# Kernel optimization log

Hardware: AMD Instinct MI355X
Metric: run time of the kernel (lower is better)

## Reference

```python
import jax, jax.numpy as jnp
import numpy as np


def gatv2(x, src, dst, ea, Wl, bl, Wr, br, We, att, bias, N):
    # PyG GATv2Conv: source/target projections, edge embedding, leaky_relu(0.2)
    # attention, segment softmax over incoming edges, scatter-add aggregation.
    H, C = att.shape
    xl = (x @ Wl.T + bl).reshape(-1, H, C)   # [N,H,C] (source / message features)
    xr = (x @ Wr.T + br).reshape(-1, H, C)   # [N,H,C] (target features)
    ee = (ea @ We.T).reshape(-1, H, C)       # [E,H,C] edge embedding
    e = jax.nn.leaky_relu(xl[src] + xr[dst] + ee, 0.2)   # [E,H,C]
    s = jnp.einsum('ehc,hc->eh', e, att)                  # [E,H] scores
    smax = jax.ops.segment_max(s, dst, num_segments=N)
    ex = jnp.exp(s - smax[dst])
    den = jax.ops.segment_sum(ex, dst, num_segments=N)
    a = ex / (den[dst] + 1e-16)                           # segment softmax
    out = jax.ops.segment_sum(a[:, :, None] * xl[src], dst, num_segments=N)
    return out.reshape(N, H * C) + bias


def _forward(x, edge_index, edge_attr, actions, Wl1, bl1, Wr1, br1, We1, att1, bias1,
             Wl2, bl2, Wr2, br2, We2, att2, bias2, Wf, bf, Wp, bp, alpha):
    N = x.shape[0]
    E = edge_attr.shape[0]
    num_actions = E + 1
    src, dst = edge_index[0], edge_index[1]
    # add_self_loops(fill_value='mean'): self-loop edge_attr = per-node mean of incoming edge_attr
    cnt = jax.ops.segment_sum(jnp.ones((E,), x.dtype), dst, num_segments=N)
    mean_ea = jax.ops.segment_sum(edge_attr, dst, num_segments=N) / jnp.maximum(cnt, 1.0)[:, None]
    loop = jnp.arange(N, dtype=src.dtype)
    src2 = jnp.concatenate([src, loop])
    dst2 = jnp.concatenate([dst, loop])
    ea2 = jnp.concatenate([edge_attr, mean_ea], axis=0)
    h = jax.nn.relu(gatv2(x, src2, dst2, ea2, Wl1, bl1, Wr1, br1, We1, att1, bias1, N))
    h = jax.nn.relu(gatv2(h, src2, dst2, ea2, Wl2, bl2, Wr2, br2, We2, att2, bias2, N))
    g = jnp.mean(h, axis=0, keepdims=True)              # global_mean_pool, single graph -> [1,hid]
    state_potential = jax.nn.relu(g @ Wp.T + bp)[:, 0]  # [1]
    diag = jnp.concatenate([src != dst, jnp.array([True])])  # [E+1]
    logits = (g @ Wf.T + bf)[:, :num_actions]           # [1, E+1]
    amask = jnp.ones((num_actions,), bool).at[actions].set(False)
    mask = amask & diag
    logits = jnp.where(mask[None, :], logits, -jnp.inf)
    return jax.nn.softmax(logits, axis=1), state_potential, jax.nn.sigmoid(alpha)


def setup_inputs() -> dict:
    key = jax.random.key(0)
    ks = jax.random.split(key, 16)
    N, E, F, hid, H, A = 20000, 400000, 128, 64, 4, 450000
    x = jax.random.normal(ks[0], (N, F), jnp.float32)
    src = jax.random.randint(ks[1], (E,), 0, N)
    dst = (src + 1 + jax.random.randint(ks[2], (E,), 0, N - 1)) % N  # no pre-existing self loops
    edge_index = jnp.stack([src, dst])
    edge_attr = jax.random.normal(ks[3], (E, 1), jnp.float32)
    actions = jax.random.randint(ks[4], (128,), 0, E + 1)
    s = 0.05
    nrm = lambda k, shp: jax.random.normal(k, shp, jnp.float32) * s
    return {
        'x': x, 'edge_index': edge_index, 'edge_attr': edge_attr, 'actions': actions,
        'Wl1': nrm(ks[5], (H * hid, F)), 'bl1': jnp.zeros(H * hid),
        'Wr1': nrm(ks[6], (H * hid, F)), 'br1': jnp.zeros(H * hid),
        'We1': nrm(ks[7], (H * hid, 1)), 'att1': nrm(ks[8], (H, hid)), 'bias1': jnp.zeros(H * hid),
        'Wl2': nrm(ks[9], (hid, H * hid)), 'bl2': jnp.zeros(hid),
        'Wr2': nrm(ks[10], (hid, H * hid)), 'br2': jnp.zeros(hid),
        'We2': nrm(ks[11], (hid, 1)), 'att2': nrm(ks[12], (1, hid)), 'bias2': jnp.zeros(hid),
        'Wf': nrm(ks[13], (A, hid)), 'bf': jnp.zeros(A),
        'Wp': nrm(ks[14], (1, hid)), 'bp': jnp.zeros(1),
        'alpha': jnp.asarray(0.0, jnp.float32),
    }


def reference(x, edge_index, edge_attr, actions, Wl1, bl1, Wr1, br1, We1, att1, bias1,
              Wl2, bl2, Wr2, br2, We2, att2, bias2, Wf, bf, Wp, bp, alpha):
    return _forward(x, edge_index, edge_attr, actions, Wl1, bl1, Wr1, br1, We1, att1, bias1,
                    Wl2, bl2, Wr2, br2, We2, att2, bias2, Wf, bf, Wp, bp, alpha)
```

## Files before the change

kernel.cpp:

```cpp
#include <hip/hip_runtime.h>
#include <math.h>

typedef __attribute__((ext_vector_type(8))) short short8;
typedef __attribute__((ext_vector_type(4))) float f32x4;

__device__ __forceinline__ float wred_sum(float v) {
#pragma unroll
  for (int off = 32; off; off >>= 1) v += __shfl_xor(v, off, 64);
  return v;
}
__device__ __forceinline__ float wred_max(float v) {
#pragma unroll
  for (int off = 32; off; off >>= 1) v = fmaxf(v, __shfl_xor(v, off, 64));
  return v;
}
__device__ __forceinline__ unsigned f2key(float x) {
  unsigned b = __float_as_uint(x);
  return (b & 0x80000000u) ? ~b : (b | 0x80000000u);
}
__device__ __forceinline__ float key2f(unsigned k) {
  unsigned b = (k & 0x80000000u) ? (k & 0x7FFFFFFFu) : ~k;
  return __uint_as_float(b);
}
__device__ __forceinline__ float b2f(unsigned short u) {
  return __uint_as_float(((unsigned)u) << 16);
}
__device__ __forceinline__ unsigned short f2b(float f) {
  unsigned b = __float_as_uint(f);
  return (unsigned short)((b + 0x7FFFu + ((b >> 16) & 1u)) >> 16);
}

__global__ __launch_bounds__(256) void k_prep(
    const float* __restrict__ s0, ushort* __restrict__ d0, int n0,
    const float* __restrict__ s1, ushort* __restrict__ d1, int n1,
    const float* __restrict__ s2, ushort* __restrict__ d2, int n2,
    const float* __restrict__ s3, ushort* __restrict__ d3, int n3,
    const float* __restrict__ s4, ushort* __restrict__ d4, int n4,
    const int* __restrict__ dstv, const float* __restrict__ ea,
    int* __restrict__ cnt_i, float* __restrict__ sum_ea, int E,
    const int* __restrict__ actions, unsigned char* __restrict__ aflag,
    int n_act, int castB) {
  int b = blockIdx.x, tid = threadIdx.x;
  if (b == 0 && tid < n_act) aflag[actions[tid]] = 1;
  if (b < castB) {
    int t = (b * 256 + tid) * 4;
    const float* s; ushort* d; int off = t;
    if (off < n0) { s = s0; d = d0; }
    else { off -= n0;
      if (off < n1) { s = s1; d = d1; }
      else { off -= n1;
        if (off < n2) { s = s2; d = d2; }
        else { off -= n2;
          if (off < n3) { s = s3; d = d3; }
          else { off -= n3;
            if (off < n4) { s = s4; d = d4; }
            else return; } } } }
    float4 v = *(const float4*)(s + off);
    ushort4 o;
    o.x = f2b(v.x); o.y = f2b(v.y); o.z = f2b(v.z); o.w = f2b(v.w);
    *(ushort4*)(d + off) = o;
    return;
  }
  int e = (b - castB) * 256 + tid;
  if (e >= E) return;
  int d = dstv[e];
  atomicAdd(&cnt_i[d], 1);
  atomicAdd(&sum_ea[d], ea[e]);
}

__global__ __launch_bounds__(1024) void k_scan(const int* __restrict__ cnt_i,
    const float* __restrict__ sum_ea, float* __restrict__ mean_ea,
    int* __restrict__ row_st, int* __restrict__ cursor, int N) {
  __shared__ int ws[16];
  int tid = threadIdx.x;
  int lane = tid & 63, w = tid >> 6;
  int running = 0;
  for (int base = 0; base < N; base += 1024) {
    int i = base + tid;
    int c = 0;
    if (i < N) {
      int cc = cnt_i[i];
      c = cc + 1;
      mean_ea[i] = sum_ea[i] / fmaxf((float)cc, 1.0f);
    }
    int inc = c;
#pragma unroll
    for (int off = 1; off < 64; off <<= 1) {
      int u = __shfl_up(inc, off, 64);
      if (lane >= off) inc += u;
    }
    if (lane == 63) ws[w] = inc;
    __syncthreads();
    if (tid < 16) {
      int s = ws[tid];
#pragma unroll
      for (int off = 1; off < 16; off <<= 1) {
        int u = __shfl_up(s, off, 16);
        if (tid >= off) s += u;
      }
      ws[tid] = s;
    }
    __syncthreads();
    int woff = (w == 0) ? 0 : ws[w - 1];
    int total = ws[15];
    int ex = running + woff + (inc - c);
    if (i < N) { row_st[i] = ex; cursor[i] = ex; }
    running += total;
    __syncthreads();
  }
  if (tid == 0) row_st[N] = running;
}

__global__ __launch_bounds__(256) void k_gemm_scatter(const ushort* __restrict__ A,
    const ushort* __restrict__ W0, const float* __restrict__ b0, ushort* __restrict__ C0,
    const ushort* __restrict__ W1, const float* __restrict__ b1, ushort* __restrict__ C1,
    int M, int Nc, int K,
    const int* __restrict__ dstv, const int* __restrict__ srcv,
    const float* __restrict__ ea, const float* __restrict__ mean_ea,
    int* __restrict__ cursor, int* __restrict__ srcp, float* __restrict__ eap,
    int E, int E2) {
  int tid = threadIdx.x;
  if (blockIdx.z == 2) {
    int flat = blockIdx.x * gridDim.y + blockIdx.y;
    int stride = gridDim.x * gridDim.y * 256;
    for (int e = flat * 256 + tid; e < E2; e += stride) {
      int d, sn; float av;
      if (e < E) { d = dstv[e]; sn = srcv[e]; av = ea[e]; }
      else { d = e - E; sn = d; av = mean_ea[d]; }
      int pos = atomicAdd(&cursor[d], 1);
      srcp[pos] = sn;
      eap[pos] = av;
    }
    return;
  }
  const ushort* W = blockIdx.z ? W1 : W0;
  const float* bias = blockIdx.z ? b1 : b0;
  ushort* C = blockIdx.z ? C1 : C0;
  int wave = tid >> 6, lane = tid & 63;
  int m0 = blockIdx.x * 64 + wave * 16;
  int n0 = blockIdx.y * 64;
  int r = lane & 15, g = lane >> 4;
  f32x4 acc[4] = {};
  int am = min(m0 + r, M - 1);
  const ushort* Arow = A + (size_t)am * K + g * 8;
  const ushort* Wrow = W + (size_t)(n0 + r) * K + g * 8;
  for (int k0 = 0; k0 < K; k0 += 32) {
    short8 a = *(const short8*)(const void*)(Arow + k0);
#pragma unroll
    for (int c = 0; c < 4; ++c) {
      short8 b = *(const short8*)(const void*)(Wrow + (size_t)c * 16 * K + k0);
      acc[c] = __builtin_amdgcn_mfma_f32_16x16x32_bf16(a, b, acc[c], 0, 0, 0);
    }
  }
#pragma unroll
  for (int c = 0; c < 4; ++c) {
    int gn = n0 + c * 16 + r;
    float bv = bias[gn];
#pragma unroll
    for (int j = 0; j < 4; ++j) {
      int gm = m0 + g * 4 + j;
      if (gm < M) C[(size_t)gm * Nc + gn] = f2b(acc[c][j] + bv);
    }
  }
}

__global__ __launch_bounds__(256) void k_gemm_mfma2(const ushort* __restrict__ A,
    const ushort* __restrict__ W0, const float* __restrict__ b0, ushort* __restrict__ C0,
    const ushort* __restrict__ W1, const float* __restrict__ b1, ushort* __restrict__ C1,
    int M, int Nc, int K) {
  const ushort* W = blockIdx.z ? W1 : W0;
  const float* bias = blockIdx.z ? b1 : b0;
  ushort* C = blockIdx.z ? C1 : C0;
  int wave = threadIdx.x >> 6, lane = threadIdx.x & 63;
  int m0 = blockIdx.x * 64 + wave * 16;
  int n0 = blockIdx.y * 64;
  int r = lane & 15, g = lane >> 4;
  f32x4 acc[4] = {};
  int am = min(m0 + r, M - 1);
  const ushort* Arow = A + (size_t)am * K + g * 8;
  const ushort* Wrow = W + (size_t)(n0 + r) * K + g * 8;
  for (int k0 = 0; k0 < K; k0 += 32) {
    short8 a = *(const short8*)(const void*)(Arow + k0);
#pragma unroll
    for (int c = 0; c < 4; ++c) {
      short8 b = *(const short8*)(const void*)(Wrow + (size_t)c * 16 * K + k0);
      acc[c] = __builtin_amdgcn_mfma_f32_16x16x32_bf16(a, b, acc[c], 0, 0, 0);
    }
  }
#pragma unroll
  for (int c = 0; c < 4; ++c) {
    int gn = n0 + c * 16 + r;
    float bv = bias[gn];
#pragma unroll
    for (int j = 0; j < 4; ++j) {
      int gm = m0 + g * 4 + j;
      if (gm < M) C[(size_t)gm * Nc + gn] = f2b(acc[c][j] + bv);
    }
  }
}

__global__ __launch_bounds__(256) void k_fused1(const ushort* __restrict__ xl,
    const ushort* __restrict__ xr, const int* __restrict__ srcp,
    const float* __restrict__ eap, const int* __restrict__ row_st,
    const float* __restrict__ We, const float* __restrict__ att,
    const float* __restrict__ bias, ushort* __restrict__ out, int N) {
  int tid = threadIdx.x;
  int lane = tid & 63;
  int half = lane >> 5, l32 = lane & 31;
  int n = blockIdx.x * 8 + (tid >> 6) * 2 + half;
  if (n >= N) return;
  int c0 = l32 * 8;
  float4 Wa = *(const float4*)(We + c0), Wb = *(const float4*)(We + c0 + 4);
  float4 Aa = *(const float4*)(att + c0), Ab = *(const float4*)(att + c0 + 4);
  float Wev[8] = {Wa.x, Wa.y, Wa.z, Wa.w, Wb.x, Wb.y, Wb.z, Wb.w};
  float atv[8] = {Aa.x, Aa.y, Aa.z, Aa.w, Ab.x, Ab.y, Ab.z, Ab.w};
  short8 xru = *(const short8*)(const void*)(xr + (size_t)n * 256 + c0);
  float xrf[8];
#pragma unroll
  for (int j = 0; j < 8; ++j) xrf[j] = b2f((unsigned short)xru[j]);
  int a = row_st[n], b = row_st[n + 1];
  float m = -INFINITY, den = 0.f;
  float acc[8] = {};
  int sn_nx = srcp[a];
  float av_nx = eap[a];
  for (int i = a; i < b; ++i) {
    int sn = sn_nx;
    float av = av_nx;
    short8 xu = *(const short8*)(const void*)(xl + (size_t)sn * 256 + c0);
    if (i + 1 < b) { sn_nx = srcp[i + 1]; av_nx = eap[i + 1]; }
    float x[8];
    float t = 0.f;
#pragma unroll
    for (int j = 0; j < 8; ++j) {
      x[j] = b2f((unsigned short)xu[j]);
      float v = x[j] + xrf[j] + av * Wev[j];
      v = v > 0.f ? v : 0.2f * v;
      t += atv[j] * v;
    }
    t += __shfl_xor(t, 1, 8);
    t += __shfl_xor(t, 2, 8);
    t += __shfl_xor(t, 4, 8);
    if (t > m) {
      float sc = __expf(m - t);
      m = t; den *= sc;
#pragma unroll
      for (int j = 0; j < 8; ++j) acc[j] *= sc;
    }
    float ex = __expf(t - m);
    den += ex;
#pragma unroll
    for (int j = 0; j < 8; ++j) acc[j] += ex * x[j];
  }
  float inv = 1.f / (den + 1e-16f);
  float4 Ba = *(const float4*)(bias + c0), Bb = *(const float4*)(bias + c0 + 4);
  float bv[8] = {Ba.x, Ba.y, Ba.z, Ba.w, Bb.x, Bb.y, Bb.z, Bb.w};
  short8 o;
#pragma unroll
  for (int j = 0; j < 8; ++j) o[j] = (short)f2b(fmaxf(acc[j] * inv + bv[j], 0.f));
  *(short8*)(void*)(out + (size_t)n * 256 + c0) = o;
}

__global__ __launch_bounds__(256) void k_fused2(const ushort* __restrict__ xl,
    const ushort* __restrict__ xr, const int* __restrict__ srcp,
    const float* __restrict__ eap, const int* __restrict__ row_st,
    const float* __restrict__ We, const float* __restrict__ att,
    const float* __restrict__ bias, float* __restrict__ g_sum, int N) {
  __shared__ float gred[4][64];
  int tid = threadIdx.x;
  int lane = tid & 63, w = tid >> 6;
  int sub = lane >> 3, l8 = lane & 7;
  int n = blockIdx.x * 32 + w * 8 + sub;
  bool valid = n < N;
  int c0 = l8 * 8;
  float4 Wa = *(const float4*)(We + c0), Wb = *(const float4*)(We + c0 + 4);
  float4 Aa = *(const float4*)(att + c0), Ab = *(const float4*)(att + c0 + 4);
  float Wev[8] = {Wa.x, Wa.y, Wa.z, Wa.w, Wb.x, Wb.y, Wb.z, Wb.w};
  float atv[8] = {Aa.x, Aa.y, Aa.z, Aa.w, Ab.x, Ab.y, Ab.z, Ab.w};
  float xrf[8] = {};
  if (valid) {
    short8 xru = *(const short8*)(const void*)(xr + (size_t)n * 64 + c0);
#pragma unroll
    for (int j = 0; j < 8; ++j) xrf[j] = b2f((unsigned short)xru[j]);
  }
  int a = 0, b = 0;
  if (valid) { a = row_st[n]; b = row_st[n + 1]; }
  float m = -INFINITY, den = 0.f;
  float acc[8] = {};
  int sn_nx = valid ? srcp[a] : 0;
  float av_nx = valid ? eap[a] : 0.f;
  for (int i = a; i < b; ++i) {
    int sn = sn_nx;
    float av = av_nx;
    short8 xu = *(const short8*)(const void*)(xl + (size_t)sn * 64 + c0);
    if (i + 1 < b) { sn_nx = srcp[i + 1]; av_nx = eap[i + 1]; }
    float x[8];
    float t = 0.f;
#pragma unroll
    for (int j = 0; j < 8; ++j) {
      x[j] = b2f((unsigned short)xu[j]);
      float v = x[j] + xrf[j] + av * Wev[j];
      v = v > 0.f ? v : 0.2f * v;
      t += atv[j] * v;
    }
    t += __shfl_xor(t, 1, 8);
    t += __shfl_xor(t, 2, 8);
    t += __shfl_xor(t, 4, 8);
    if (t > m) {
      float sc = __expf(m - t);
      m = t; den *= sc;
#pragma unroll
      for (int j = 0; j < 8; ++j) acc[j] *= sc;
    }
    float ex = __expf(t - m);
    den += ex;
#pragma unroll
    for (int j = 0; j < 8; ++j) acc[j] += ex * x[j];
  }
  float inv = 1.f / (den + 1e-16f);
  float4 Ba = *(const float4*)(bias + c0), Bb = *(const float4*)(bias + c0 + 4);
  float bv[8] = {Ba.x, Ba.y, Ba.z, Ba.w, Bb.x, Bb.y, Bb.z, Bb.w};
  float vals[8];
#pragma unroll
  for (int j = 0; j < 8; ++j)
    vals[j] = valid ? fmaxf(acc[j] * inv + bv[j], 0.f) : 0.f;
#pragma unroll
  for (int j = 0; j < 8; ++j) {
    float v = vals[j];
    v += __shfl_xor(v, 8, 64);
    v += __shfl_xor(v, 16, 64);
    v += __shfl_xor(v, 32, 64);
    vals[j] = v;
  }
  if (lane < 8) {
#pragma unroll
    for (int j = 0; j < 8; ++j) gred[w][lane * 8 + j] = vals[j];
  }
  __syncthreads();
  if (tid < 64)
    atomicAdd(&g_sum[tid], gred[0][tid] + gred[1][tid] + gred[2][tid] + gred[3][tid]);
}

__global__ __launch_bounds__(256) void k_logits(const float* __restrict__ g_sum,
    const float* __restrict__ Wp, const float* __restrict__ bp,
    const float* __restrict__ alpha,
    const float* __restrict__ Wf, const float* __restrict__ bf,
    const unsigned char* __restrict__ aflag, const int* __restrict__ src,
    const int* __restrict__ dst, float* __restrict__ logits,
    unsigned* __restrict__ gmax_key, float* __restrict__ out,
    int E, int NA, float invN) {
  __shared__ float gs[64];
  __shared__ float wmax[4];
  int tid = threadIdx.x;
  if (tid < 64) gs[tid] = g_sum[tid] * invN;
  __syncthreads();
  if (blockIdx.x == 0 && tid < 64) {
    float t = wred_sum(gs[tid] * Wp[tid]);
    if (tid == 0) {
      float sp = t + bp[0];
      out[NA] = sp > 0.f ? sp : 0.f;
      out[NA + 1] = 1.f / (1.f + __expf(-alpha[0]));
    }
  }
  int j0 = tid & 3;
  int row = blockIdx.x * 64 + (tid >> 2);
  float val = -INFINITY;
  if (row < NA) {
    const float4* wr = (const float4*)(Wf + (size_t)row * 64);
    const float4* g4 = (const float4*)gs;
    float acc = 0.f;
#pragma unroll
    for (int u = 0; u < 4; ++u) {
      float4 w = wr[j0 + u * 4];
      float4 gv = g4[j0 + u * 4];
      acc += w.x * gv.x + w.y * gv.y + w.z * gv.z + w.w * gv.w;
    }
    acc += __shfl_xor(acc, 1, 4);
    acc += __shfl_xor(acc, 2, 4);
    if (j0 == 0) {
      bool keep = (!aflag[row]) && (row >= E || src[row] != dst[row]);
      val = keep ? (acc + bf[row]) : -INFINITY;
      logits[row] = val;
    }
  }
  float mv = wred_max(val);
  if ((tid & 63) == 0) wmax[tid >> 6] = mv;
  __syncthreads();
  if (tid == 0) {
    float m = fmaxf(fmaxf(wmax[0], wmax[1]), fmaxf(wmax[2], wmax[3]));
    atomicMax(&gmax_key[blockIdx.x & 63], f2key(m));
  }
}

__global__ __launch_bounds__(256) void k_exp(float* __restrict__ logits,
    const unsigned* __restrict__ gmax_key, float* __restrict__ gsum, int NA) {
  __shared__ float wsum[4];
  int tid = threadIdx.x;
  float gmax = key2f(gmax_key[tid & 63]);
  gmax = wred_max(gmax);
  int i = (blockIdx.x * 256 + tid) * 4;
  float s = 0.f;
  if (i < NA) {
    float4 v = *(const float4*)(logits + i);
    float4 e;
    e.x = (i + 0 < NA && v.x != -INFINITY) ? __expf(v.x - gmax) : 0.f;
    e.y = (i + 1 < NA && v.y != -INFINITY) ? __expf(v.y - gmax) : 0.f;
    e.z = (i + 2 < NA && v.z != -INFINITY) ? __expf(v.z - gmax) : 0.f;
    e.w = (i + 3 < NA && v.w != -INFINITY) ? __expf(v.w - gmax) : 0.f;
    *(float4*)(logits + i) = e;
    s = e.x + e.y + e.z + e.w;
  }
  s = wred_sum(s);
  if ((tid & 63) == 0) wsum[tid >> 6] = s;
  __syncthreads();
  if (tid == 0)
    atomicAdd(gsum, wsum[0] + wsum[1] + wsum[2] + wsum[3]);
}

__global__ __launch_bounds__(256) void k_norm(const float* __restrict__ logits,
    const float* __restrict__ gsum, float* __restrict__ out, int NA) {
  int i = (blockIdx.x * 256 + threadIdx.x) * 4;
  if (i >= NA) return;
  float inv = 1.f / (*gsum);
  if (i + 3 < NA) {
    float4 v = *(const float4*)(logits + i);
    float4 o;
    o.x = v.x * inv; o.y = v.y * inv; o.z = v.z * inv; o.w = v.w * inv;
    *(float4*)(out + i) = o;
  } else {
    for (int j = i; j < NA; ++j) out[j] = logits[j] * inv;
  }
}

extern "C" void kernel_launch(void* const* d_in, const int* in_sizes, int n_in,
                              void* d_out, int out_size, void* d_ws, size_t ws_size,
                              hipStream_t stream) {
  const float* x      = (const float*)d_in[0];
  const int*   eidx   = (const int*)d_in[1];
  const float* eattr  = (const float*)d_in[2];
  const int*   actions= (const int*)d_in[3];
  const float* Wl1 = (const float*)d_in[4];
  const float* bl1 = (const float*)d_in[5];
  const float* Wr1 = (const float*)d_in[6];
  const float* br1 = (const float*)d_in[7];
  const float* We1 = (const float*)d_in[8];
  const float* att1= (const float*)d_in[9];
  const float* bias1=(const float*)d_in[10];
  const float* Wl2 = (const float*)d_in[11];
  const float* bl2 = (const float*)d_in[12];
  const float* Wr2 = (const float*)d_in[13];
  const float* br2 = (const float*)d_in[14];
  const float* We2 = (const float*)d_in[15];
  const float* att2= (const float*)d_in[16];
  const float* bias2=(const float*)d_in[17];
  const float* Wf  = (const float*)d_in[18];
  const float* bf  = (const float*)d_in[19];
  const float* Wp  = (const float*)d_in[20];
  const float* bp  = (const float*)d_in[21];
  const float* alpha=(const float*)d_in[22];

  const int F = 128;
  const int N = in_sizes[0] / F;
  const int E = in_sizes[2];
  const int E2 = E + N;
  const int NA = E + 1;
  const int n_act = in_sizes[3];
  const int* src = eidx;
  const int* dst = eidx + E;

  float* ws = (float*)d_ws;
  size_t p = 0;
  int*      cnt_i    = (int*)(ws + p);      p += (size_t)N;
  float*    sum_ea   = ws + p;              p += (size_t)N;
  float*    g_sum    = ws + p;              p += 64;
  unsigned* gmax_key = (unsigned*)(ws + p); p += 64;
  float*    gsum     = ws + p;              p += 64;
  unsigned char* aflag = (unsigned char*)(ws + p); p += ((size_t)NA + 3) / 4;
  size_t zero_bytes = p * sizeof(float);
  float*    mean_ea  = ws + p;              p += (size_t)N;
  int*      row_st   = (int*)(ws + p);      p += (size_t)N + 64;
  int*      cursor   = (int*)(ws + p);      p += (size_t)N;
  int*      srcp     = (int*)(ws + p);      p += (size_t)E2;
  float*    eap      = ws + p;              p += (size_t)E2;
  float*    logits   = ws + p;              p += (size_t)NA + 64;
  p = (p + 3) & ~(size_t)3;
  ushort* ub = (ushort*)(ws + p);
  size_t q = 0;
  ushort* xb   = ub + q; q += (size_t)N * F;
  ushort* wl1b = ub + q; q += (size_t)256 * 128;
  ushort* wr1b = ub + q; q += (size_t)256 * 128;
  ushort* wl2b = ub + q; q += (size_t)64 * 256;
  ushort* wr2b = ub + q; q += (size_t)64 * 256;
  ushort* xl1b = ub + q; q += (size_t)N * 256;
  ushort* xr1b = ub + q; q += (size_t)N * 256;
  ushort* h1b  = ub + q; q += (size_t)N * 256;
  ushort* xl2b = ub + q; q += (size_t)N * 64;
  ushort* xr2b = ub + q; q += (size_t)N * 64;

  float* out = (float*)d_out;

  hipMemsetAsync(d_ws, 0, zero_bytes, stream);

  {
    int n0 = N * F, n1 = 256 * 128, n2 = 256 * 128, n3 = 64 * 256, n4 = 64 * 256;
    int tot4 = (n0 + n1 + n2 + n3 + n4) / 4;
    int castB = (tot4 + 255) / 256;
    int cntB = (E + 255) / 256;
    k_prep<<<castB + cntB, 256, 0, stream>>>(
        x, xb, n0, Wl1, wl1b, n1, Wr1, wr1b, n2, Wl2, wl2b, n3, Wr2, wr2b, n4,
        dst, eattr, cnt_i, sum_ea, E, actions, aflag, n_act, castB);
  }

  k_scan<<<1, 1024, 0, stream>>>(cnt_i, sum_ea, mean_ea, row_st, cursor, N);

  {
    dim3 g1((N + 63) / 64, 4, 3);
    k_gemm_scatter<<<g1, 256, 0, stream>>>(xb, wl1b, bl1, xl1b, wr1b, br1, xr1b,
                                           N, 256, 128,
                                           dst, src, eattr, mean_ea, cursor,
                                           srcp, eap, E, E2);
  }
  k_fused1<<<(N + 7) / 8, 256, 0, stream>>>(xl1b, xr1b, srcp, eap, row_st,
                                            We1, att1, bias1, h1b, N);
  {
    dim3 g2((N + 63) / 64, 1, 2);
    k_gemm_mfma2<<<g2, 256, 0, stream>>>(h1b, wl2b, bl2, xl2b, wr2b, br2, xr2b,
                                         N, 64, 256);
  }
  k_fused2<<<(N + 31) / 32, 256, 0, stream>>>(xl2b, xr2b, srcp, eap, row_st,
                                              We2, att2, bias2, g_sum, N);

  k_logits<<<(NA + 63) / 64, 256, 0, stream>>>(
      g_sum, Wp, bp, alpha, Wf, bf, aflag, src, dst,
      logits, gmax_key, out, E, NA, 1.0f / (float)N);
  int nb4 = (NA + 1023) / 1024;
  k_exp<<<nb4, 256, 0, stream>>>(logits, gmax_key, gsum, NA);
  k_norm<<<nb4, 256, 0, stream>>>(logits, gsum, out, NA);
}
```

Measured before the change: 272.0 us.

## Fold CSR scan into the GEMM launch and unroll edge loops by two

The standalone single-block scan kernel is removed. The prefix sum now runs as an extra z-slice of the first GEMM launch, using a 256-thread serial-chunk scan, and the mean of edge_attr is computed on the fly. Edge scatter becomes its own one-thread-per-edge kernel. Both fused attention kernels now process two edges per iteration, issuing two gathers at once and doing one online-softmax rescale per pair, to raise memory-level parallelism. The cost is a serial per-thread chunk scan with strided accesses and slightly more register use.

```diff
diff --git a/kernel.cpp b/kernel.cpp
--- a/kernel.cpp
+++ b/kernel.cpp
@@ -68,69 +68,37 @@
   atomicAdd(&sum_ea[d], ea[e]);
 }
 
-__global__ __launch_bounds__(1024) void k_scan(const int* __restrict__ cnt_i,
-    const float* __restrict__ sum_ea, float* __restrict__ mean_ea,
-    int* __restrict__ row_st, int* __restrict__ cursor, int N) {
-  __shared__ int ws[16];
+__global__ __launch_bounds__(256) void k_gemm_scan(const ushort* __restrict__ A,
+    const ushort* __restrict__ W0, const float* __restrict__ b0, ushort* __restrict__ C0,
+    const ushort* __restrict__ W1, const float* __restrict__ b1, ushort* __restrict__ C1,
+    int M, int Nc, int K,
+    const int* __restrict__ cnt_i, int* __restrict__ row_st,
+    int* __restrict__ cursor, int N) {
   int tid = threadIdx.x;
-  int lane = tid & 63, w = tid >> 6;
-  int running = 0;
-  for (int base = 0; base < N; base += 1024) {
-    int i = base + tid;
-    int c = 0;
-    if (i < N) {
-      int cc = cnt_i[i];
-      c = cc + 1;
-      mean_ea[i] = sum_ea[i] / fmaxf((float)cc, 1.0f);
-    }
-    int inc = c;
+  if (blockIdx.z == 2) {
+    if (blockIdx.x != 0 || blockIdx.y != 0) return;
+    __shared__ int wtot[4];
+    int per = (N + 255) / 256;
+    int begin = tid * per, end = min(begin + per, N);
+    int s = 0;
+    for (int idx = begin; idx < end; ++idx) s += cnt_i[idx] + 1;
+    int lane = tid & 63, w = tid >> 6;
+    int inc = s;
 #pragma unroll
     for (int off = 1; off < 64; off <<= 1) {
       int u = __shfl_up(inc, off, 64);
       if (lane >= off) inc += u;
     }
-    if (lane == 63) ws[w] = inc;
+    if (lane == 63) wtot[w] = inc;
     __syncthreads();
-    if (tid < 16) {
-      int s = ws[tid];
-#pragma unroll
-      for (int off = 1; off < 16; off <<= 1) {
-        int u = __shfl_up(s, off, 16);
-        if (tid >= off) s += u;
-      }
-      ws[tid] = s;
-    }
-    __syncthreads();
-    int woff = (w == 0) ? 0 : ws[w - 1];
-    int total = ws[15];
-    int ex = running + woff + (inc - c);
-    if (i < N) { row_st[i] = ex; cursor[i] = ex; }
-    running += total;
-    __syncthreads();
-  }
-  if (tid == 0) row_st[N] = running;
-}
-
-__global__ __launch_bounds__(256) void k_gemm_scatter(const ushort* __restrict__ A,
-    const ushort* __restrict__ W0, const float* __restrict__ b0, ushort* __restrict__ C0,
-    const ushort* __restrict__ W1, const float* __restrict__ b1, ushort* __restrict__ C1,
-    int M, int Nc, int K,
-    const int* __restrict__ dstv, const int* __restrict__ srcv,
-    const float* __restrict__ ea, const float* __restrict__ mean_ea,
-    int* __restrict__ cursor, int* __restrict__ srcp, float* __restrict__ eap,
-    int E, int E2) {
-  int tid = threadIdx.x;
-  if (blockIdx.z == 2) {
-    int flat = blockIdx.x * gridDim.y + blockIdx.y;
-    int stride = gridDim.x * gridDim.y * 256;
-    for (int e = flat * 256 + tid; e < E2; e += stride) {
-      int d, sn; float av;
-      if (e < E) { d = dstv[e]; sn = srcv[e]; av = ea[e]; }
-      else { d = e - E; sn = d; av = mean_ea[d]; }
-      int pos = atomicAdd(&cursor[d], 1);
-      srcp[pos] = sn;
-      eap[pos] = av;
-    }
+    int woff = 0;
+    for (int k = 0; k < w; ++k) woff += wtot[k];
+    int run = woff + inc - s;
+    for (int idx = begin; idx < end; ++idx) {
+      row_st[idx] = run; cursor[idx] = run;
+      run += cnt_i[idx] + 1;
+    }
+    if (tid == 255) row_st[N] = run;
     return;
   }
   const ushort* W = blockIdx.z ? W1 : W0;
@@ -162,6 +130,21 @@
       if (gm < M) C[(size_t)gm * Nc + gn] = f2b(acc[c][j] + bv);
     }
   }
+}
+
+__global__ __launch_bounds__(256) void k_scatter(const int* __restrict__ dstv,
+    const int* __restrict__ srcv, const float* __restrict__ ea,
+    const int* __restrict__ cnt_i, const float* __restrict__ sum_ea,
+    int* __restrict__ cursor, int* __restrict__ srcp, float* __restrict__ eap,
+    int E, int E2) {
+  int e = blockIdx.x * 256 + threadIdx.x;
+  if (e >= E2) return;
+  int d, sn; float av;
+  if (e < E) { d = dstv[e]; sn = srcv[e]; av = ea[e]; }
+  else { d = e - E; sn = d; av = sum_ea[d] / fmaxf((float)cnt_i[d], 1.0f); }
+  int pos = atomicAdd(&cursor[d], 1);
+  srcp[pos] = sn;
+  eap[pos] = av;
 }
 
 __global__ __launch_bounds__(256) void k_gemm_mfma2(const ushort* __restrict__ A,
@@ -221,13 +204,44 @@
   int a = row_st[n], b = row_st[n + 1];
   float m = -INFINITY, den = 0.f;
   float acc[8] = {};
-  int sn_nx = srcp[a];
-  float av_nx = eap[a];
-  for (int i = a; i < b; ++i) {
-    int sn = sn_nx;
-    float av = av_nx;
+  int i = a;
+  for (; i + 1 < b; i += 2) {
+    int sn0 = srcp[i], sn1 = srcp[i + 1];
+    float av0 = eap[i], av1 = eap[i + 1];
+    short8 xu0 = *(const short8*)(const void*)(xl + (size_t)sn0 * 256 + c0);
+    short8 xu1 = *(const short8*)(const void*)(xl + (size_t)sn1 * 256 + c0);
+    float x0[8], x1[8];
+    float t0 = 0.f, t1 = 0.f;
+#pragma unroll
+    for (int j = 0; j < 8; ++j) {
+      x0[j] = b2f((unsigned short)xu0[j]);
+      x1[j] = b2f((unsigned short)xu1[j]);
+      float v0 = x0[j] + xrf[j] + av0 * Wev[j];
+      float v1 = x1[j] + xrf[j] + av1 * Wev[j];
+      v0 = v0 > 0.f ? v0 : 0.2f * v0;
+      v1 = v1 > 0.f ? v1 : 0.2f * v1;
+      t0 += atv[j] * v0;
+      t1 += atv[j] * v1;
+    }
+    t0 += __shfl_xor(t0, 1, 8); t1 += __shfl_xor(t1, 1, 8);
+    t0 += __shfl_xor(t0, 2, 8); t1 += __shfl_xor(t1, 2, 8);
+    t0 += __shfl_xor(t0, 4, 8); t1 += __shfl_xor(t1, 4, 8);
+    float tm = fmaxf(t0, t1);
+    if (tm > m) {
+      float sc = __expf(m - tm);
+      m = tm; den *= sc;
+#pragma unroll
+      for (int j = 0; j < 8; ++j) acc[j] *= sc;
+    }
+    float e0 = __expf(t0 - m), e1 = __expf(t1 - m);
+    den += e0 + e1;
+#pragma unroll
+    for (int j = 0; j < 8; ++j) acc[j] += e0 * x0[j] + e1 * x1[j];
+  }
+  if (i < b) {
+    int sn = srcp[i];
+    float av = eap[i];
     short8 xu = *(const short8*)(const void*)(xl + (size_t)sn * 256 + c0);
-    if (i + 1 < b) { sn_nx = srcp[i + 1]; av_nx = eap[i + 1]; }
     float x[8];
     float t = 0.f;
 #pragma unroll
@@ -286,13 +300,44 @@
   if (valid) { a = row_st[n]; b = row_st[n + 1]; }
   float m = -INFINITY, den = 0.f;
   float acc[8] = {};
-  int sn_nx = valid ? srcp[a] : 0;
-  float av_nx = valid ? eap[a] : 0.f;
-  for (int i = a; i < b; ++i) {
-    int sn = sn_nx;
-    float av = av_nx;
+  int i = a;
+  for (; i + 1 < b; i += 2) {
+    int sn0 = srcp[i], sn1 = srcp[i + 1];
+    float av0 = eap[i], av1 = eap[i + 1];
+    short8 xu0 = *(const short8*)(const void*)(xl + (size_t)sn0 * 64 + c0);
+    short8 xu1 = *(const short8*)(const void*)(xl + (size_t)sn1 * 64 + c0);
+    float x0[8], x1[8];
+    float t0 = 0.f, t1 = 0.f;
+#pragma unroll
+    for (int j = 0; j < 8; ++j) {
+      x0[j] = b2f((unsigned short)xu0[j]);
+      x1[j] = b2f((unsigned short)xu1[j]);
+      float v0 = x0[j] + xrf[j] + av0 * Wev[j];
+      float v1 = x1[j] + xrf[j] + av1 * Wev[j];
+      v0 = v0 > 0.f ? v0 : 0.2f * v0;
+      v1 = v1 > 0.f ? v1 : 0.2f * v1;
+      t0 += atv[j] * v0;
+      t1 += atv[j] * v1;
+    }
+    t0 += __shfl_xor(t0, 1, 8); t1 += __shfl_xor(t1, 1, 8);
+    t0 += __shfl_xor(t0, 2, 8); t1 += __shfl_xor(t1, 2, 8);
+    t0 += __shfl_xor(t0, 4, 8); t1 += __shfl_xor(t1, 4, 8);
+    float tm = fmaxf(t0, t1);
+    if (tm > m) {
+      float sc = __expf(m - tm);
+      m = tm; den *= sc;
+#pragma unroll
+      for (int j = 0; j < 8; ++j) acc[j] *= sc;
+    }
+    float e0 = __expf(t0 - m), e1 = __expf(t1 - m);
+    den += e0 + e1;
+#pragma unroll
+    for (int j = 0; j < 8; ++j) acc[j] += e0 * x0[j] + e1 * x1[j];
+  }
+  if (i < b) {
+    int sn = srcp[i];
+    float av = eap[i];
     short8 xu = *(const short8*)(const void*)(xl + (size_t)sn * 64 + c0);
-    if (i + 1 < b) { sn_nx = srcp[i + 1]; av_nx = eap[i + 1]; }
     float x[8];
     float t = 0.f;
 #pragma unroll
@@ -476,7 +521,6 @@
   float*    gsum     = ws + p;              p += 64;
   unsigned char* aflag = (unsigned char*)(ws + p); p += ((size_t)NA + 3) / 4;
   size_t zero_bytes = p * sizeof(float);
-  float*    mean_ea  = ws + p;              p += (size_t)N;
   int*      row_st   = (int*)(ws + p);      p += (size_t)N + 64;
   int*      cursor   = (int*)(ws + p);      p += (size_t)N;
   int*      srcp     = (int*)(ws + p);      p += (size_t)E2;
@@ -510,15 +554,13 @@
         dst, eattr, cnt_i, sum_ea, E, actions, aflag, n_act, castB);
   }
 
-  k_scan<<<1, 1024, 0, stream>>>(cnt_i, sum_ea, mean_ea, row_st, cursor, N);
-
   {
     dim3 g1((N + 63) / 64, 4, 3);
-    k_gemm_scatter<<<g1, 256, 0, stream>>>(xb, wl1b, bl1, xl1b, wr1b, br1, xr1b,
-                                           N, 256, 128,
-                                           dst, src, eattr, mean_ea, cursor,
-                                           srcp, eap, E, E2);
-  }
+    k_gemm_scan<<<g1, 256, 0, stream>>>(xb, wl1b, bl1, xl1b, wr1b, br1, xr1b,
+                                        N, 256, 128, cnt_i, row_st, cursor, N);
+  }
+  k_scatter<<<(E2 + 255) / 256, 256, 0, stream>>>(dst, src, eattr, cnt_i, sum_ea,
+                                                  cursor, srcp, eap, E, E2);
   k_fused1<<<(N + 7) / 8, 256, 0, stream>>>(xl1b, xr1b, srcp, eap, row_st,
                                             We1, att1, bias1, h1b, N);
   {
```

After: 294.3 us. 1.08x slower.
